# Kernel tuning notes

Measured on AMD Instinct MI355X. Metric: run time of the kernel, lower is better.

## Reference

```python
import jax, jax.numpy as jnp
import numpy as np

B, T, D = 4, 2048, 1024  # batch, seq, latent_dim == attn_dim
H = 16                   # n_heads
HS = D // H              # head_size = 64
FF = 4 * D               # ffn hidden
EPS = 1e-5


def layernorm(x, g, b):
    mu = jnp.mean(x, axis=-1, keepdims=True)
    var = jnp.mean(jnp.square(x - mu), axis=-1, keepdims=True)
    return (x - mu) * jax.lax.rsqrt(var + EPS) * g + b


def setup_inputs() -> dict:
    key = jax.random.key(0)
    ks = jax.random.split(key, 12)
    s = lambda fan_in: 1.0 / np.sqrt(fan_in)
    return {
        "x": jax.random.normal(ks[0], (B, T, D), dtype=jnp.float32),
        "ln1_g": jnp.ones((D,), jnp.float32),
        "ln1_b": jnp.zeros((D,), jnp.float32),
        "W_ap": jax.random.normal(ks[1], (D, D), jnp.float32) * s(D),
        "b_ap": jnp.zeros((D,), jnp.float32),
        "W_qkv": jax.random.normal(ks[2], (D, 3 * D), jnp.float32) * s(D),
        "b_qkv": jnp.zeros((3 * D,), jnp.float32),
        "W_proj": jax.random.normal(ks[3], (D, D), jnp.float32) * s(D),
        "b_proj": jnp.zeros((D,), jnp.float32),
        "ln2_g": jnp.ones((D,), jnp.float32),
        "ln2_b": jnp.zeros((D,), jnp.float32),
        "W1": jax.random.normal(ks[4], (D, FF), jnp.float32) * s(D),
        "b1": jnp.zeros((FF,), jnp.float32),
        "W2": jax.random.normal(ks[5], (FF, D), jnp.float32) * s(FF),
        "b2": jnp.zeros((D,), jnp.float32),
    }


def block_fwd(x, ln1_g, ln1_b, W_ap, b_ap, W_qkv, b_qkv, W_proj, b_proj,
              ln2_g, ln2_b, W1, b1, W2, b2):
    # --- self attention branch ---
    a = layernorm(x, ln1_g, ln1_b)
    a = a @ W_ap + b_ap                       # [B,T,D]
    qkv = a @ W_qkv + b_qkv                   # [B,T,3D]
    q, k, v = jnp.split(qkv, 3, axis=-1)
    q = q.reshape(B, T, H, HS).transpose(0, 2, 1, 3)  # [B,H,T,HS]
    k = k.reshape(B, T, H, HS).transpose(0, 2, 1, 3)
    v = v.reshape(B, T, H, HS).transpose(0, 2, 1, 3)
    scores = jnp.einsum('bhqd,bhkd->bhqk', q, k) * (1.0 / np.sqrt(HS))
    probs = jax.nn.softmax(scores, axis=-1)   # full [B,H,T,T], no causal mask (as in source)
    o = jnp.einsum('bhqk,bhkd->bhqd', probs, v)
    o = o.transpose(0, 2, 1, 3).reshape(B, T, D)
    o = o @ W_proj + b_proj
    h = x + o
    # --- ffn branch: GELU(LayerNorm(h)) -> Linear -> GELU -> Linear ---
    f = jax.nn.gelu(layernorm(h, ln2_g, ln2_b), approximate=False)
    f = jax.nn.gelu(f @ W1 + b1, approximate=False) @ W2 + b2
    return h + f


def reference(x, ln1_g, ln1_b, W_ap, b_ap, W_qkv, b_qkv, W_proj, b_proj,
              ln2_g, ln2_b, W1, b1, W2, b2):
    return block_fwd(x, ln1_g, ln1_b, W_ap, b_ap, W_qkv, b_qkv, W_proj, b_proj,
                     ln2_g, ln2_b, W1, b1, W2, b2)
```

## Files before the change

kernel.cpp:

```cpp
#include <hip/hip_runtime.h>
#include <hip/hip_bf16.h>
#include <math.h>


typedef unsigned short u16;
typedef __attribute__((ext_vector_type(8))) short s16x8;
typedef __attribute__((ext_vector_type(4))) float f32x4;

__device__ __forceinline__ u16 f2bf(float f) {
    unsigned u = __float_as_uint(f);
    u += 0x7fffu + ((u >> 16) & 1u);
    return (u16)(u >> 16);
}
__device__ __forceinline__ unsigned pkbf2(float a, float b) {
    float2 t; t.x = a; t.y = b;
    __hip_bfloat162 r = __float22bfloat162_rn(t);
    return *(unsigned*)&r;
}
__device__ __forceinline__ float bf2f(short s) {
    return __uint_as_float(((unsigned)(unsigned short)s) << 16);
}
__device__ __forceinline__ float gelu_f(float v) {
    float u = v * v;
    float x = v * fmaf(0.0356774081f, u, 0.7978845608f);
    float t = __builtin_amdgcn_exp2f(x * 2.885390082f);
    float th = fmaf(-2.0f, __builtin_amdgcn_rcpf(t + 1.0f), 1.0f);
    float hv = 0.5f * v;
    return fmaf(hv, th, hv);
}
__device__ __forceinline__ void glds16(const u16* g, u16* l) {
    __builtin_amdgcn_global_load_lds(
        (const __attribute__((address_space(1))) void*)g,
        (__attribute__((address_space(3))) void*)l, 16, 0, 0);
}
__device__ __forceinline__ void barfence() {
    __builtin_amdgcn_s_barrier();
    asm volatile("" ::: "memory");
}

__global__ __launch_bounds__(256) void transpose_f32_bf16(
    const float* __restrict__ in, u16* __restrict__ out, int K, int N) {
    __shared__ float t[32][33];
    int n0 = blockIdx.x * 32, k0 = blockIdx.y * 32;
    int c = threadIdx.x, r0 = threadIdx.y;
#pragma unroll
    for (int i = 0; i < 4; i++) {
        int r = r0 + i * 8;
        t[r][c] = in[(size_t)(k0 + r) * N + n0 + c];
    }
    __syncthreads();
#pragma unroll
    for (int i = 0; i < 4; i++) {
        int r = r0 + i * 8;
        out[(size_t)(n0 + r) * K + k0 + c] = f2bf(t[c][r]);
    }
}

template <bool GELU>
__global__ __launch_bounds__(256) void ln_kernel(
    const float* __restrict__ x, const float* __restrict__ g,
    const float* __restrict__ bt, u16* __restrict__ out) {
    const int D = 1024;
    int row = blockIdx.x;
    float4 v = reinterpret_cast<const float4*>(x + (size_t)row * D)[threadIdx.x];
    float s = v.x + v.y + v.z + v.w;
    float s2 = v.x * v.x + v.y * v.y + v.z * v.z + v.w * v.w;
#pragma unroll
    for (int off = 32; off > 0; off >>= 1) {
        s += __shfl_down(s, off);
        s2 += __shfl_down(s2, off);
    }
    __shared__ float red[8];
    int wid = threadIdx.x >> 6;
    if ((threadIdx.x & 63) == 0) { red[wid] = s; red[wid + 4] = s2; }
    __syncthreads();
    s = red[0] + red[1] + red[2] + red[3];
    s2 = red[4] + red[5] + red[6] + red[7];
    float mu = s * (1.0f / 1024.0f);
    float var = s2 * (1.0f / 1024.0f) - mu * mu;
    float rstd = rsqrtf(var + 1e-5f);
    float4 gg = reinterpret_cast<const float4*>(g)[threadIdx.x];
    float4 bb = reinterpret_cast<const float4*>(bt)[threadIdx.x];
    float o0 = (v.x - mu) * rstd * gg.x + bb.x;
    float o1 = (v.y - mu) * rstd * gg.y + bb.y;
    float o2 = (v.z - mu) * rstd * gg.z + bb.z;
    float o3 = (v.w - mu) * rstd * gg.w + bb.w;
    if (GELU) { o0 = gelu_f(o0); o1 = gelu_f(o1); o2 = gelu_f(o2); o3 = gelu_f(o3); }
    uint2 o;
    o.x = pkbf2(o0, o1); o.y = pkbf2(o2, o3);
    reinterpret_cast<uint2*>(out + (size_t)row * D)[threadIdx.x] = o;
}

template <int OUT_BF16, int ACT_GELU, int HAS_RES, int SPLIT_V>
__global__ __launch_bounds__(512, 2) void gemm_kernel(
    const u16* __restrict__ A, const u16* __restrict__ BT,
    const float* __restrict__ bias, const float* __restrict__ res,
    void* __restrict__ outp, u16* __restrict__ vtg, int M, int N, int K) {
    __shared__ u16 As[2 * 256 * 64];
    __shared__ u16 Bs[2 * 256 * 64];
    const int nwg = gridDim.x * gridDim.y;
    int wg = blockIdx.y * gridDim.x + blockIdx.x;
    wg = (wg & 7) * (nwg >> 3) + (wg >> 3);
    const int m0 = (wg / gridDim.x) * 256, n0 = (wg % gridDim.x) * 256;
    const int tid = threadIdx.x;
    const int w = tid >> 6, lane = tid & 63, l16 = lane & 15, quad = lane >> 4;
    const int wm = w >> 2, wn = w & 3;

    const int lrow = lane >> 3;
    const int lcol = ((lane & 7) ^ lrow) * 8;
    const u16* Ag = A + (size_t)(m0 + w * 16 + lrow) * K + lcol;
    const u16* Bg = BT + (size_t)(n0 + w * 16 + lrow) * K + lcol;

    const int cx0 = (quad ^ (l16 & 7)) * 8;
    const int cx1 = cx0 ^ 32;

    f32x4 acc[2][2][4][2] = {};
    const int nt = K >> 6;

#define STAGE_A(AH, BUF, KK)                                              \
    do {                                                                  \
        const u16* _s = Ag + (size_t)((AH) * 128) * K + (KK);             \
        u16* _d = As + (BUF) * 16384 + ((AH) * 128 + w * 16) * 64;        \
        glds16(_s, _d);                                                   \
        glds16(_s + (size_t)8 * K, _d + 512);                             \
    } while (0)
#define STAGE_B(BH, BUF, KK)                                              \
    do {                                                                  \
        const u16* _s = Bg + (size_t)((BH) * 128) * K + (KK);             \
        u16* _d = Bs + (BUF) * 16384 + ((BH) * 128 + w * 16) * 64;        \
        glds16(_s, _d);                                                   \
        glds16(_s + (size_t)8 * K, _d + 512);                             \
    } while (0)

    STAGE_A(0, 0, 0);
    STAGE_B(0, 0, 0);
    STAGE_A(1, 0, 0);
    STAGE_B(1, 0, 0);
    asm volatile("s_waitcnt vmcnt(4)" ::: "memory");
    barfence();

    s16x8 af[4][2], bfA[2][2], bfB[2][2];

    for (int t = 0; t < nt; ++t) {
        const int cur = t & 1, nxt = cur ^ 1;
        const int kk = (t + 1) << 6;
        const bool pre = (t + 1) < nt;
        const u16* Ab = As + cur * 16384;
        const u16* Bb = Bs + cur * 16384;

#pragma unroll
        for (int i = 0; i < 4; ++i) {
            const u16* p = Ab + (wm * 64 + i * 16 + l16) * 64;
            af[i][0] = *(const s16x8*)(p + cx0);
            af[i][1] = *(const s16x8*)(p + cx1);
        }
#pragma unroll
        for (int j = 0; j < 2; ++j) {
            const u16* p = Bb + (wn * 32 + j * 16 + l16) * 64;
            bfA[j][0] = *(const s16x8*)(p + cx0);
            bfA[j][1] = *(const s16x8*)(p + cx1);
        }
        if (pre) STAGE_A(0, nxt, kk);
        barfence();
        asm volatile("s_waitcnt lgkmcnt(0)" ::: "memory");
        __builtin_amdgcn_sched_barrier(0);
        __builtin_amdgcn_s_setprio(1);
#pragma unroll
        for (int kd = 0; kd < 2; ++kd)
#pragma unroll
            for (int i = 0; i < 4; ++i)
#pragma unroll
                for (int j = 0; j < 2; ++j)
                    acc[0][0][i][j] = __builtin_amdgcn_mfma_f32_16x16x32_bf16(
                        af[i][kd], bfA[j][kd], acc[0][0][i][j], 0, 0, 0);
        __builtin_amdgcn_s_setprio(0);
        if (pre) asm volatile("s_waitcnt vmcnt(4)" ::: "memory");
        else     asm volatile("s_waitcnt vmcnt(2)" ::: "memory");
        barfence();

#pragma unroll
        for (int i = 0; i < 4; ++i) {
            const u16* p = Ab + (128 + wm * 64 + i * 16 + l16) * 64;
            af[i][0] = *(const s16x8*)(p + cx0);
            af[i][1] = *(const s16x8*)(p + cx1);
        }
        if (pre) STAGE_B(0, nxt, kk);
        barfence();
        asm volatile("s_waitcnt lgkmcnt(0)" ::: "memory");
        __builtin_amdgcn_sched_barrier(0);
        __builtin_amdgcn_s_setprio(1);
#pragma unroll
        for (int kd = 0; kd < 2; ++kd)
#pragma unroll
            for (int i = 0; i < 4; ++i)
#pragma unroll
                for (int j = 0; j < 2; ++j)
                    acc[1][0][i][j] = __builtin_amdgcn_mfma_f32_16x16x32_bf16(
                        af[i][kd], bfA[j][kd], acc[1][0][i][j], 0, 0, 0);
        __builtin_amdgcn_s_setprio(0);
        if (pre) asm volatile("s_waitcnt vmcnt(4)" ::: "memory");
        else     asm volatile("s_waitcnt vmcnt(0)" ::: "memory");
        barfence();

#pragma unroll
        for (int j = 0; j < 2; ++j) {
            const u16* p = Bb + (128 + wn * 32 + j * 16 + l16) * 64;
            bfB[j][0] = *(const s16x8*)(p + cx0);
            bfB[j][1] = *(const s16x8*)(p + cx1);
        }
        if (pre) STAGE_A(1, nxt, kk);
        barfence();
        asm volatile("s_waitcnt lgkmcnt(0)" ::: "memory");
        __builtin_amdgcn_sched_barrier(0);
        __builtin_amdgcn_s_setprio(1);
#pragma unroll
        for (int kd = 0; kd < 2; ++kd)
#pragma unroll
            for (int i = 0; i < 4; ++i)
#pragma unroll
                for (int j = 0; j < 2; ++j)
                    acc[1][1][i][j] = __builtin_amdgcn_mfma_f32_16x16x32_bf16(
                        af[i][kd], bfB[j][kd], acc[1][1][i][j], 0, 0, 0);
        __builtin_amdgcn_s_setprio(0);
        asm volatile("" ::: "memory");
        barfence();

#pragma unroll
        for (int i = 0; i < 4; ++i) {
            const u16* p = Ab + (wm * 64 + i * 16 + l16) * 64;
            af[i][0] = *(const s16x8*)(p + cx0);
            af[i][1] = *(const s16x8*)(p + cx1);
        }
        if (pre) STAGE_B(1, nxt, kk);
        barfence();
        asm volatile("s_waitcnt lgkmcnt(0)" ::: "memory");
        __builtin_amdgcn_sched_barrier(0);
        __builtin_amdgcn_s_setprio(1);
#pragma unroll
        for (int kd = 0; kd < 2; ++kd)
#pragma unroll
            for (int i = 0; i < 4; ++i)
#pragma unroll
                for (int j = 0; j < 2; ++j)
                    acc[0][1][i][j] = __builtin_amdgcn_mfma_f32_16x16x32_bf16(
                        af[i][kd], bfB[j][kd], acc[0][1][i][j], 0, 0, 0);
        __builtin_amdgcn_s_setprio(0);
        if (pre) {
            asm volatile("s_waitcnt vmcnt(4)" ::: "memory");
            barfence();
        }
    }
#undef STAGE_A
#undef STAGE_B

    float bv[2][2];
#pragma unroll
    for (int bh = 0; bh < 2; ++bh)
#pragma unroll
        for (int j = 0; j < 2; ++j)
            bv[bh][j] = bias[n0 + bh * 128 + wn * 32 + j * 16 + l16];

    if (SPLIT_V && n0 >= 2048) {
#pragma unroll
        for (int ah = 0; ah < 2; ++ah)
#pragma unroll
            for (int i = 0; i < 4; ++i) {
                int rowb = m0 + ah * 128 + wm * 64 + i * 16 + quad * 4;
                int bb = rowb >> 11, tt = rowb & 2047;
#pragma unroll
                for (int bh = 0; bh < 2; ++bh)
#pragma unroll
                    for (int j = 0; j < 2; ++j) {
                        int vcol = n0 + bh * 128 + wn * 32 + j * 16 + l16 - 2048;
                        uint2 pk;
                        pk.x = pkbf2(acc[ah][bh][i][j][0] + bv[bh][j],
                                     acc[ah][bh][i][j][1] + bv[bh][j]);
                        pk.y = pkbf2(acc[ah][bh][i][j][2] + bv[bh][j],
                                     acc[ah][bh][i][j][3] + bv[bh][j]);
                        *(uint2*)&vtg[((size_t)bb * 1024 + vcol) * 2048 + tt] = pk;
                    }
            }
    } else {
#pragma unroll
        for (int ah = 0; ah < 2; ++ah)
#pragma unroll
            for (int i = 0; i < 4; ++i) {
                int rowb = m0 + ah * 128 + wm * 64 + i * 16 + quad * 4;
#pragma unroll
                for (int bh = 0; bh < 2; ++bh)
#pragma unroll
                    for (int j = 0; j < 2; ++j) {
                        int col = n0 + bh * 128 + wn * 32 + j * 16 + l16;
#pragma unroll
                        for (int r = 0; r < 4; ++r) {
                            float v = acc[ah][bh][i][j][r] + bv[bh][j];
                            if (ACT_GELU) v = gelu_f(v);
                            size_t idx = (size_t)(rowb + r) * N + col;
                            if (HAS_RES) v += res[idx];
                            if (OUT_BF16) ((u16*)outp)[idx] = f2bf(v);
                            else          ((float*)outp)[idx] = v;
                        }
                    }
            }
    }
}

__global__ __launch_bounds__(256) void knorm_kernel(
    const u16* __restrict__ qkv, float* __restrict__ maxkn) {
    const int T = 2048, D3 = 3072;
    int bh = blockIdx.x, b = bh >> 4, h = bh & 15;
    const u16* kg = qkv + (size_t)b * T * D3 + 1024 + h * 64;
    float mx = 0.f;
#pragma unroll
    for (int i = 0; i < 8; i++) {
        const u16* kp = kg + (size_t)(threadIdx.x + i * 256) * D3;
        float ss = 0.f;
#pragma unroll
        for (int c = 0; c < 8; c++) {
            s16x8 v = *(const s16x8*)(kp + c * 8);
#pragma unroll
            for (int j = 0; j < 8; j++) { float f = bf2f(v[j]); ss = fmaf(f, f, ss); }
        }
        mx = fmaxf(mx, ss);
    }
#pragma unroll
    for (int off = 32; off > 0; off >>= 1) mx = fmaxf(mx, __shfl_down(mx, off));
    __shared__ float red[4];
    if ((threadIdx.x & 63) == 0) red[threadIdx.x >> 6] = mx;
    __syncthreads();
    if (threadIdx.x == 0)
        maxkn[bh] = sqrtf(fmaxf(fmaxf(red[0], red[1]), fmaxf(red[2], red[3])));
}

__global__ __launch_bounds__(256, 4) void attn_kernel(
    const u16* __restrict__ qkv, const u16* __restrict__ vtg,
    const float* __restrict__ maxkn, u16* __restrict__ o) {
    const int T = 2048, D3 = 3072, Dm = 1024;
    const int bh = blockIdx.x, qb = blockIdx.y;
    const int b = bh >> 4, h = bh & 15;
    const int tid = threadIdx.x;
    const int w = tid >> 6, lane = tid & 63, l16 = lane & 15, quad = lane >> 4;
    const size_t tokbase = (size_t)b * T;
    const float s2 = 0.125f * 1.44269504088896f;

    __shared__ u16 Ks[64 * 72];
    __shared__ u16 Vts[64 * 72];
    __shared__ u16 Pt[4][32 * 72];

    s16x8 bq[2][2];
    float m2[2];
    const float kn = maxkn[bh];
#pragma unroll
    for (int qs = 0; qs < 2; qs++) {
        int qrow = qb * 128 + w * 32 + qs * 16 + l16;
        const u16* qp = qkv + (tokbase + qrow) * D3 + h * 64 + quad * 8;
        bq[qs][0] = *(const s16x8*)qp;
        bq[qs][1] = *(const s16x8*)(qp + 32);
        float ss = 0.f;
#pragma unroll
        for (int kd = 0; kd < 2; kd++)
#pragma unroll
            for (int j = 0; j < 8; j++) {
                float v = bf2f(bq[qs][kd][j]); ss = fmaf(v, v, ss);
            }
        ss += __shfl_xor(ss, 16);
        ss += __shfl_xor(ss, 32);
        m2[qs] = sqrtf(ss) * kn * s2;
    }

    f32x4 acc_ot[2][4] = {};
    float lp[2] = {0.f, 0.f};

    const u16* kgbase = qkv + tokbase * D3 + 1024 + h * 64;
    const u16* vgbase = vtg + ((size_t)b * 1024 + h * 64) * T;

    const int srow = tid >> 3;
    const int scv = (tid & 7) * 8;

    for (int kt = 0; kt < 32; kt++) {
        __syncthreads();
#pragma unroll
        for (int s = 0; s < 2; s++) {
            int row = srow + s * 32;
            *(s16x8*)&Ks[row * 72 + scv] =
                *(const s16x8*)(kgbase + (size_t)(kt * 64 + row) * D3 + scv);
            *(s16x8*)&Vts[row * 72 + scv] =
                *(const s16x8*)(vgbase + (size_t)row * T + kt * 64 + scv);
        }
        __syncthreads();

        f32x4 st[2][4] = {};
#pragma unroll
        for (int kd = 0; kd < 2; kd++)
#pragma unroll
            for (int kb = 0; kb < 4; kb++) {
                s16x8 ak = *(const s16x8*)&Ks[(kb * 16 + l16) * 72 + kd * 32 + quad * 8];
#pragma unroll
                for (int qs = 0; qs < 2; qs++)
                    st[qs][kb] = __builtin_amdgcn_mfma_f32_16x16x32_bf16(
                        ak, bq[qs][kd], st[qs][kb], 0, 0, 0);
            }

#pragma unroll
        for (int qs = 0; qs < 2; qs++) {
            float acc_l = 0.f;
#pragma unroll
            for (int kb = 0; kb < 4; kb++) {
#pragma unroll
                for (int r = 0; r < 4; r++) {
                    float pv = __builtin_amdgcn_exp2f(fmaf(st[qs][kb][r], s2, -m2[qs]));
                    st[qs][kb][r] = pv;
                    acc_l += pv;
                }
                uint2 pk;
                pk.x = pkbf2(st[qs][kb][0], st[qs][kb][1]);
                pk.y = pkbf2(st[qs][kb][2], st[qs][kb][3]);
                *(uint2*)&Pt[w][(qs * 16 + l16) * 72 + kb * 16 + quad * 4] = pk;
            }
            lp[qs] += acc_l;
        }

#pragma unroll
        for (int kk = 0; kk < 2; kk++) {
            s16x8 bp[2];
#pragma unroll
            for (int qs = 0; qs < 2; qs++)
                bp[qs] = *(const s16x8*)&Pt[w][(qs * 16 + l16) * 72 + kk * 32 + quad * 8];
#pragma unroll
            for (int dt = 0; dt < 4; dt++) {
                s16x8 av = *(const s16x8*)&Vts[(dt * 16 + l16) * 72 + kk * 32 + quad * 8];
#pragma unroll
                for (int qs = 0; qs < 2; qs++)
                    acc_ot[qs][dt] = __builtin_amdgcn_mfma_f32_16x16x32_bf16(
                        av, bp[qs], acc_ot[qs][dt], 0, 0, 0);
            }
        }
    }

#pragma unroll
    for (int qs = 0; qs < 2; qs++) {
        float l = lp[qs];
        l += __shfl_xor(l, 16);
        l += __shfl_xor(l, 32);
        float inv = 1.0f / l;
        int token = qb * 128 + w * 32 + qs * 16 + l16;
#pragma unroll
        for (int dt = 0; dt < 4; dt++) {
            uint2 pk;
            pk.x = pkbf2(acc_ot[qs][dt][0] * inv, acc_ot[qs][dt][1] * inv);
            pk.y = pkbf2(acc_ot[qs][dt][2] * inv, acc_ot[qs][dt][3] * inv);
            *(uint2*)&o[(tokbase + token) * Dm + h * 64 + dt * 16 + quad * 4] = pk;
        }
    }
}

extern "C" void kernel_launch(void* const* d_in, const int* in_sizes, int n_in,
                              void* d_out, int out_size, void* d_ws, size_t ws_size,
                              hipStream_t stream) {
    const int M = 8192;
    const int D = 1024, D3 = 3072, FF = 4096;

    const float* x      = (const float*)d_in[0];
    const float* ln1_g  = (const float*)d_in[1];
    const float* ln1_b  = (const float*)d_in[2];
    const float* W_ap   = (const float*)d_in[3];
    const float* b_ap   = (const float*)d_in[4];
    const float* W_qkv  = (const float*)d_in[5];
    const float* b_qkv  = (const float*)d_in[6];
    const float* W_proj = (const float*)d_in[7];
    const float* b_proj = (const float*)d_in[8];
    const float* ln2_g  = (const float*)d_in[9];
    const float* ln2_b  = (const float*)d_in[10];
    const float* W1     = (const float*)d_in[11];
    const float* b1     = (const float*)d_in[12];
    const float* W2     = (const float*)d_in[13];
    const float* b2     = (const float*)d_in[14];

    char* p = (char*)d_ws;
    auto carve = [&](size_t bytes) { char* r = p; p += (bytes + 255) & ~(size_t)255; return r; };
    u16*   WapT   = (u16*)carve((size_t)D * D * 2);
    u16*   WqkvT  = (u16*)carve((size_t)D * D3 * 2);
    u16*   WprojT = (u16*)carve((size_t)D * D * 2);
    u16*   W1T    = (u16*)carve((size_t)D * FF * 2);
    u16*   W2T    = (u16*)carve((size_t)FF * D * 2);
    u16*   aln    = (u16*)carve((size_t)M * D * 2);
    u16*   a1     = (u16*)carve((size_t)M * D * 2);
    u16*   qkvb   = (u16*)carve((size_t)M * D3 * 2);
    float* hbuf   = (float*)carve((size_t)M * D * 4);
    u16*   f1     = (u16*)carve((size_t)M * FF * 2);
    float* maxkn  = (float*)carve(64 * 4);
    u16* gbuf = aln;
    u16* obuf = a1;
    u16* vtg  = f1;

    dim3 tb(32, 8);
    transpose_f32_bf16<<<dim3(D / 32, D / 32), tb, 0, stream>>>(W_ap, WapT, D, D);
    transpose_f32_bf16<<<dim3(D3 / 32, D / 32), tb, 0, stream>>>(W_qkv, WqkvT, D, D3);
    transpose_f32_bf16<<<dim3(D / 32, D / 32), tb, 0, stream>>>(W_proj, WprojT, D, D);
    transpose_f32_bf16<<<dim3(FF / 32, D / 32), tb, 0, stream>>>(W1, W1T, D, FF);
    transpose_f32_bf16<<<dim3(D / 32, FF / 32), tb, 0, stream>>>(W2, W2T, FF, D);

    ln_kernel<false><<<M, 256, 0, stream>>>(x, ln1_g, ln1_b, aln);
    gemm_kernel<1, 0, 0, 0><<<dim3(D / 256, M / 256), 512, 0, stream>>>(
        aln, WapT, b_ap, nullptr, a1, nullptr, M, D, D);
    gemm_kernel<1, 0, 0, 1><<<dim3(D3 / 256, M / 256), 512, 0, stream>>>(
        a1, WqkvT, b_qkv, nullptr, qkvb, vtg, M, D3, D);
    knorm_kernel<<<64, 256, 0, stream>>>(qkvb, maxkn);
    attn_kernel<<<dim3(64, 16), 256, 0, stream>>>(qkvb, vtg, maxkn, obuf);
    gemm_kernel<0, 0, 1, 0><<<dim3(D / 256, M / 256), 512, 0, stream>>>(
        obuf, WprojT, b_proj, x, hbuf, nullptr, M, D, D);
    ln_kernel<true><<<M, 256, 0, stream>>>(hbuf, ln2_g, ln2_b, gbuf);
    gemm_kernel<1, 1, 0, 0><<<dim3(FF / 256, M / 256), 512, 0, stream>>>(
        gbuf, W1T, b1, nullptr, f1, nullptr, M, FF, D);
    gemm_kernel<0, 0, 1, 0><<<dim3(D / 256, M / 256), 512, 0, stream>>>(
        f1, W2T, b2, hbuf, (float*)d_out, nullptr, M, D, FF);
}
```

Baseline: 612.2 us.

## Add 256x128 triple-buffered GEMM for N=1024 layers and reorder main GEMM phases

```diff
diff --git a/kernel.cpp b/kernel.cpp
--- a/kernel.cpp
+++ b/kernel.cpp
@@ -134,8 +134,8 @@
 
     STAGE_A(0, 0, 0);
     STAGE_B(0, 0, 0);
+    STAGE_B(1, 0, 0);
     STAGE_A(1, 0, 0);
-    STAGE_B(1, 0, 0);
     asm volatile("s_waitcnt vmcnt(4)" ::: "memory");
     barfence();
 
@@ -179,36 +179,36 @@
         barfence();
 
 #pragma unroll
+        for (int j = 0; j < 2; ++j) {
+            const u16* p = Bb + (128 + wn * 32 + j * 16 + l16) * 64;
+            bfB[j][0] = *(const s16x8*)(p + cx0);
+            bfB[j][1] = *(const s16x8*)(p + cx1);
+        }
+        if (pre) STAGE_B(0, nxt, kk);
+        barfence();
+        asm volatile("s_waitcnt lgkmcnt(0)" ::: "memory");
+        __builtin_amdgcn_sched_barrier(0);
+        __builtin_amdgcn_s_setprio(1);
+#pragma unroll
+        for (int kd = 0; kd < 2; ++kd)
+#pragma unroll
+            for (int i = 0; i < 4; ++i)
+#pragma unroll
+                for (int j = 0; j < 2; ++j)
+                    acc[0][1][i][j] = __builtin_amdgcn_mfma_f32_16x16x32_bf16(
+                        af[i][kd], bfB[j][kd], acc[0][1][i][j], 0, 0, 0);
+        __builtin_amdgcn_s_setprio(0);
+        if (pre) asm volatile("s_waitcnt vmcnt(4)" ::: "memory");
+        else     asm volatile("s_waitcnt vmcnt(0)" ::: "memory");
+        barfence();
+
+#pragma unroll
         for (int i = 0; i < 4; ++i) {
             const u16* p = Ab + (128 + wm * 64 + i * 16 + l16) * 64;
             af[i][0] = *(const s16x8*)(p + cx0);
             af[i][1] = *(const s16x8*)(p + cx1);
         }
-        if (pre) STAGE_B(0, nxt, kk);
-        barfence();
-        asm volatile("s_waitcnt lgkmcnt(0)" ::: "memory");
-        __builtin_amdgcn_sched_barrier(0);
-        __builtin_amdgcn_s_setprio(1);
-#pragma unroll
-        for (int kd = 0; kd < 2; ++kd)
-#pragma unroll
-            for (int i = 0; i < 4; ++i)
-#pragma unroll
-                for (int j = 0; j < 2; ++j)
-                    acc[1][0][i][j] = __builtin_amdgcn_mfma_f32_16x16x32_bf16(
-                        af[i][kd], bfA[j][kd], acc[1][0][i][j], 0, 0, 0);
-        __builtin_amdgcn_s_setprio(0);
-        if (pre) asm volatile("s_waitcnt vmcnt(4)" ::: "memory");
-        else     asm volatile("s_waitcnt vmcnt(0)" ::: "memory");
-        barfence();
-
-#pragma unroll
-        for (int j = 0; j < 2; ++j) {
-            const u16* p = Bb + (128 + wn * 32 + j * 16 + l16) * 64;
-            bfB[j][0] = *(const s16x8*)(p + cx0);
-            bfB[j][1] = *(const s16x8*)(p + cx1);
-        }
-        if (pre) STAGE_A(1, nxt, kk);
+        if (pre) STAGE_B(1, nxt, kk);
         barfence();
         asm volatile("s_waitcnt lgkmcnt(0)" ::: "memory");
         __builtin_amdgcn_sched_barrier(0);
@@ -222,18 +222,9 @@
                     acc[1][1][i][j] = __builtin_amdgcn_mfma_f32_16x16x32_bf16(
                         af[i][kd], bfB[j][kd], acc[1][1][i][j], 0, 0, 0);
         __builtin_amdgcn_s_setprio(0);
-        asm volatile("" ::: "memory");
-        barfence();
-
-#pragma unroll
-        for (int i = 0; i < 4; ++i) {
-            const u16* p = Ab + (wm * 64 + i * 16 + l16) * 64;
-            af[i][0] = *(const s16x8*)(p + cx0);
-            af[i][1] = *(const s16x8*)(p + cx1);
-        }
-        if (pre) STAGE_B(1, nxt, kk);
-        barfence();
-        asm volatile("s_waitcnt lgkmcnt(0)" ::: "memory");
+        barfence();
+
+        if (pre) STAGE_A(1, nxt, kk);
         __builtin_amdgcn_sched_barrier(0);
         __builtin_amdgcn_s_setprio(1);
 #pragma unroll
@@ -242,8 +233,8 @@
             for (int i = 0; i < 4; ++i)
 #pragma unroll
                 for (int j = 0; j < 2; ++j)
-                    acc[0][1][i][j] = __builtin_amdgcn_mfma_f32_16x16x32_bf16(
-                        af[i][kd], bfB[j][kd], acc[0][1][i][j], 0, 0, 0);
+                    acc[1][0][i][j] = __builtin_amdgcn_mfma_f32_16x16x32_bf16(
+                        af[i][kd], bfA[j][kd], acc[1][0][i][j], 0, 0, 0);
         __builtin_amdgcn_s_setprio(0);
         if (pre) {
             asm volatile("s_waitcnt vmcnt(4)" ::: "memory");
@@ -302,6 +293,144 @@
                         }
                     }
             }
+    }
+}
+
+template <int OUT_BF16, int HAS_RES>
+__global__ __launch_bounds__(512, 2) void gemm_n128(
+    const u16* __restrict__ A, const u16* __restrict__ BT,
+    const float* __restrict__ bias, const float* __restrict__ res,
+    void* __restrict__ outp, int M, int N, int K) {
+    __shared__ u16 As[3 * 256 * 64];
+    __shared__ u16 Bs[3 * 128 * 64];
+    const int nwg = gridDim.x * gridDim.y;
+    int wg = blockIdx.y * gridDim.x + blockIdx.x;
+    wg = (wg & 7) * (nwg >> 3) + (wg >> 3);
+    const int m0 = (wg / gridDim.x) * 256, n0 = (wg % gridDim.x) * 128;
+    const int tid = threadIdx.x;
+    const int w = tid >> 6, lane = tid & 63, l16 = lane & 15, quad = lane >> 4;
+    const int wm = w >> 1, wn = w & 1;
+
+    const int lrow = lane >> 3;
+    const int lcol = ((lane & 7) ^ lrow) * 8;
+    const u16* Ag = A + (size_t)(m0 + w * 16 + lrow) * K + lcol;
+    const u16* Bg = BT + (size_t)(n0 + w * 16 + lrow) * K + lcol;
+
+    const int cx0 = (quad ^ (l16 & 7)) * 8;
+    const int cx1 = cx0 ^ 32;
+
+    f32x4 acc[4][4] = {};
+    const int nt = K >> 6;
+
+#define NSTAGE_A(BUF, KK)                                                 \
+    do {                                                                  \
+        const u16* _s = Ag + (KK);                                        \
+        u16* _d = As + (BUF) * 16384 + (w * 16) * 64;                     \
+        glds16(_s, _d);                                                   \
+        glds16(_s + (size_t)8 * K, _d + 512);                             \
+        glds16(_s + (size_t)128 * K, _d + 8192);                          \
+        glds16(_s + (size_t)136 * K, _d + 8192 + 512);                    \
+    } while (0)
+#define NSTAGE_B(BUF, KK)                                                 \
+    do {                                                                  \
+        const u16* _s = Bg + (KK);                                        \
+        u16* _d = Bs + (BUF) * 8192 + (w * 16) * 64;                      \
+        glds16(_s, _d);                                                   \
+        glds16(_s + (size_t)8 * K, _d + 512);                             \
+    } while (0)
+
+    NSTAGE_A(0, 0);
+    NSTAGE_B(0, 0);
+    NSTAGE_A(1, 64);
+    NSTAGE_B(1, 64);
+    asm volatile("s_waitcnt vmcnt(6)" ::: "memory");
+    barfence();
+
+    s16x8 af[4][2], bf[2][2];
+    int cur = 0, b2 = 2;
+    for (int t = 0; t < nt; ++t) {
+        const bool pre2 = (t + 2) < nt;
+        const u16* Ab = As + cur * 16384;
+        const u16* Bb = Bs + cur * 8192;
+        const int kk2 = (t + 2) << 6;
+
+#pragma unroll
+        for (int i = 0; i < 4; ++i) {
+            const u16* p = Ab + (wm * 64 + i * 16 + l16) * 64;
+            af[i][0] = *(const s16x8*)(p + cx0);
+            af[i][1] = *(const s16x8*)(p + cx1);
+        }
+#pragma unroll
+        for (int j = 0; j < 2; ++j) {
+            const u16* p = Bb + (wn * 64 + j * 16 + l16) * 64;
+            bf[j][0] = *(const s16x8*)(p + cx0);
+            bf[j][1] = *(const s16x8*)(p + cx1);
+        }
+        if (pre2) NSTAGE_A(b2, kk2);
+        barfence();
+        asm volatile("s_waitcnt lgkmcnt(0)" ::: "memory");
+        __builtin_amdgcn_sched_barrier(0);
+        __builtin_amdgcn_s_setprio(1);
+#pragma unroll
+        for (int kd = 0; kd < 2; ++kd)
+#pragma unroll
+            for (int i = 0; i < 4; ++i)
+#pragma unroll
+                for (int j = 0; j < 2; ++j)
+                    acc[i][j] = __builtin_amdgcn_mfma_f32_16x16x32_bf16(
+                        af[i][kd], bf[j][kd], acc[i][j], 0, 0, 0);
+        __builtin_amdgcn_s_setprio(0);
+        barfence();
+
+#pragma unroll
+        for (int j = 0; j < 2; ++j) {
+            const u16* p = Bb + (wn * 64 + 32 + j * 16 + l16) * 64;
+            bf[j][0] = *(const s16x8*)(p + cx0);
+            bf[j][1] = *(const s16x8*)(p + cx1);
+        }
+        if (pre2) NSTAGE_B(b2, kk2);
+        barfence();
+        asm volatile("s_waitcnt lgkmcnt(0)" ::: "memory");
+        __builtin_amdgcn_sched_barrier(0);
+        __builtin_amdgcn_s_setprio(1);
+#pragma unroll
+        for (int kd = 0; kd < 2; ++kd)
+#pragma unroll
+            for (int i = 0; i < 4; ++i)
+#pragma unroll
+                for (int j = 0; j < 2; ++j)
+                    acc[i][2 + j] = __builtin_amdgcn_mfma_f32_16x16x32_bf16(
+                        af[i][kd], bf[j][kd], acc[i][2 + j], 0, 0, 0);
+        __builtin_amdgcn_s_setprio(0);
+        if (pre2)               asm volatile("s_waitcnt vmcnt(6)" ::: "memory");
+        else if (t + 1 < nt)    asm volatile("s_waitcnt vmcnt(0)" ::: "memory");
+        if (t + 1 < nt) barfence();
+
+        cur = (cur == 2) ? 0 : cur + 1;
+        b2 = (b2 == 2) ? 0 : b2 + 1;
+    }
+#undef NSTAGE_A
+#undef NSTAGE_B
+
+    float bv[4];
+#pragma unroll
+    for (int j = 0; j < 4; ++j) bv[j] = bias[n0 + wn * 64 + j * 16 + l16];
+
+#pragma unroll
+    for (int i = 0; i < 4; ++i) {
+        int rowb = m0 + wm * 64 + i * 16 + quad * 4;
+#pragma unroll
+        for (int j = 0; j < 4; ++j) {
+            int col = n0 + wn * 64 + j * 16 + l16;
+#pragma unroll
+            for (int r = 0; r < 4; ++r) {
+                float v = acc[i][j][r] + bv[j];
+                size_t idx = (size_t)(rowb + r) * N + col;
+                if (HAS_RES) v += res[idx];
+                if (OUT_BF16) ((u16*)outp)[idx] = f2bf(v);
+                else          ((float*)outp)[idx] = v;
+            }
+        }
     }
 }
 
@@ -501,17 +630,17 @@
     transpose_f32_bf16<<<dim3(D / 32, FF / 32), tb, 0, stream>>>(W2, W2T, FF, D);
 
     ln_kernel<false><<<M, 256, 0, stream>>>(x, ln1_g, ln1_b, aln);
-    gemm_kernel<1, 0, 0, 0><<<dim3(D / 256, M / 256), 512, 0, stream>>>(
-        aln, WapT, b_ap, nullptr, a1, nullptr, M, D, D);
+    gemm_n128<1, 0><<<dim3(D / 128, M / 256), 512, 0, stream>>>(
+        aln, WapT, b_ap, nullptr, a1, M, D, D);
     gemm_kernel<1, 0, 0, 1><<<dim3(D3 / 256, M / 256), 512, 0, stream>>>(
         a1, WqkvT, b_qkv, nullptr, qkvb, vtg, M, D3, D);
     knorm_kernel<<<64, 256, 0, stream>>>(qkvb, maxkn);
     attn_kernel<<<dim3(64, 16), 256, 0, stream>>>(qkvb, vtg, maxkn, obuf);
-    gemm_kernel<0, 0, 1, 0><<<dim3(D / 256, M / 256), 512, 0, stream>>>(
-        obuf, WprojT, b_proj, x, hbuf, nullptr, M, D, D);
+    gemm_n128<0, 1><<<dim3(D / 128, M / 256), 512, 0, stream>>>(
+        obuf, WprojT, b_proj, x, hbuf, M, D, D);
     ln_kernel<true><<<M, 256, 0, stream>>>(hbuf, ln2_g, ln2_b, gbuf);
     gemm_kernel<1, 1, 0, 0><<<dim3(FF / 256, M / 256), 512, 0, stream>>>(
         gbuf, W1T, b1, nullptr, f1, nullptr, M, FF, D);
-    gemm_kernel<0, 0, 1, 0><<<dim3(D / 256, M / 256), 512, 0, stream>>>(
-        f1, W2T, b2, hbuf, (float*)d_out, nullptr, M, D, FF);
-}
+    gemm_n128<0, 1><<<dim3(D / 128, M / 256), 512, 0, stream>>>(
+        f1, W2T, b2, hbuf, (float*)d_out, M, D, FF);
+}
```

New measurement: 539.1 us. -11.9%, faster.
